# Kernel tuning notes

Measured on AMD Instinct MI355X. Metric: run time of the kernel, lower is better.

The kernel has to match this reference:

```python
import jax, jax.numpy as jnp
import numpy as np

S, T1, B = 1024, 65, 32   # source len, target len (incl. <start>), batch
E, H, V, D = 512, 512, 32000, 32  # embed, hidden, vocab, window half-width
PAD = 0


def _p(key, shape):
    return jax.random.normal(key, shape, dtype=jnp.float32) * 0.05


def setup_inputs() -> dict:
    key = jax.random.key(0)
    ks = jax.random.split(key, 16)
    return {
        "source": jax.random.randint(ks[0], (S, B), 0, V),
        "target": jax.random.randint(ks[1], (T1, B), 0, V),
        "src_emb": _p(ks[2], (V, E)),
        "tar_emb": _p(ks[3], (V, E)),
        "enc_Wih": _p(ks[4], (4 * H, E)),
        "enc_Whh": _p(ks[5], (4 * H, H)),
        "enc_b": _p(ks[6], (4 * H,)),
        "dec_Wih": _p(ks[7], (4 * H, E + H)),
        "dec_Whh": _p(ks[8], (4 * H, H)),
        "dec_b": _p(ks[9], (4 * H,)),
        "W_ht2tan": _p(ks[10], (H, H)),
        "W_tan2pt": _p(ks[11], (1, H)),
        "W_ct2ht": _p(ks[12], (H, 2 * H)),
        "W_ht2final": _p(ks[13], (V, H)),
    }


def _lstm_cell(x, h, c, Wih, Whh, b):
    g = x @ Wih.T + h @ Whh.T + b  # [B,4H], torch gate order i,f,g,o
    i, f, gg, o = jnp.split(g, 4, axis=-1)
    c = jax.nn.sigmoid(f) * c + jax.nn.sigmoid(i) * jnp.tanh(gg)
    h = jax.nn.sigmoid(o) * jnp.tanh(c)
    return h, c


def reference(source, target, src_emb, tar_emb, enc_Wih, enc_Whh, enc_b,
              dec_Wih, dec_Whh, dec_b, W_ht2tan, W_tan2pt, W_ct2ht, W_ht2final):
    # ---- encode (all lengths == S, so packing is a no-op) ----
    x = src_emb[source]  # [S,B,E]
    h0 = jnp.zeros((B, H), jnp.float32)

    def enc_step(carry, xt):
        h, c = carry
        h, c = _lstm_cell(xt, h, c, enc_Wih, enc_Whh, enc_b)
        return (h, c), h

    (hn, cn), enc_out = jax.lax.scan(enc_step, (h0, h0), x)
    encode_h = enc_out.transpose(1, 0, 2)  # [B,S,H]
    lens_f = jnp.full((B,), float(S), jnp.float32)
    pos = jnp.arange(S, dtype=jnp.float32)  # [S]

    # ---- decode ----
    y = tar_emb[target[:-1]]  # [T,B,E]

    def dec_step(carry, y_t):
        h, c, ht = carry
        x_t = jnp.concatenate([y_t, ht], axis=1)  # [B,E+H]
        h, c = _lstm_cell(x_t, h, c, dec_Wih, dec_Whh, dec_b)
        yt = h  # [B,H]
        pt = jax.nn.sigmoid(jnp.tanh(yt @ W_ht2tan.T) @ W_tan2pt.T)[:, 0]  # [B]
        center = lens_f * pt  # [B]
        ci = jnp.floor(center).astype(jnp.int32)
        left = jnp.maximum(0, ci - D)  # [B]
        right = jnp.minimum(S, ci + D)
        mask = (pos[None, :] >= left[:, None, None].squeeze(-1)) & (pos[None, :] < right[:, None])  # [B,S]
        scores = jnp.einsum('bh,bsh->bs', yt, encode_h)
        align = jax.nn.softmax(jnp.where(mask, scores, -1e30), axis=-1)
        gauss = jnp.exp(-jnp.square(pos[None, :] - center[:, None]) / (D * D / 2.0))
        at = align * gauss * mask
        ct = jnp.einsum('bs,bsh->bh', at, encode_h)
        # original computes attention under torch.no_grad()
        batch_ct = jax.lax.stop_gradient(jnp.concatenate([ct, yt], axis=1))  # [B,2H]
        ht_new = jnp.tanh(batch_ct @ W_ct2ht.T)
        return (h, c, ht_new), ht_new

    ht0 = jnp.zeros((B, H), jnp.float32)
    _, dec_out = jax.lax.scan(dec_step, (hn, cn, ht0), y)  # [T,B,H]

    P = jax.nn.log_softmax(dec_out @ W_ht2final.T, axis=-1)  # [T,B,V]
    tgt = target[1:]  # [T,B]
    tar_mask = (tgt != PAD).astype(jnp.float32)
    logp = jnp.take_along_axis(P, tgt[..., None], axis=-1)[..., 0] * tar_mask
    return logp.sum(axis=0)  # [B]
```

## Files before the change

### kernel.cpp

```cpp
#include <hip/hip_runtime.h>
#include <stdint.h>
#include <math.h>


typedef _Float16 f16;
typedef _Float16 f16x2 __attribute__((ext_vector_type(2)));
typedef _Float16 f16x4v __attribute__((ext_vector_type(4)));
typedef _Float16 f16x8v __attribute__((ext_vector_type(8)));
typedef float    f32x4v __attribute__((ext_vector_type(4)));
typedef int i32x4 __attribute__((ext_vector_type(4)));

union V8 { f16x2 p[4]; float4 f4; };

#define CH  4
#define WPC 64

__device__ __forceinline__ float dot2f(f16x2 a, f16x2 b, float c) {
#if __has_builtin(__builtin_amdgcn_fdot2)
    return __builtin_amdgcn_fdot2(a, b, c, false);
#else
    return c + (float)a[0] * (float)b[0] + (float)a[1] * (float)b[1];
#endif
}

__device__ __forceinline__ float sigf(float x) { return 1.0f / (1.0f + __expf(-x)); }

__device__ __forceinline__ float tanh_f(float x) {
    float ax = fminf(fabsf(x), 12.0f);
    float e  = __expf(2.0f * ax);
    float r  = (e - 1.0f) / (e + 1.0f);
    return copysignf(r, x);
}

__device__ __forceinline__ void st_wt_b16(f16* p, f16 v) {
    union { f16 h; uint16_t u; } cv; cv.h = v;
    uint32_t d = cv.u;
    asm volatile("global_store_short %0, %1, off sc0 sc1" :: "v"(p), "v"(d) : "memory");
}
__device__ __forceinline__ void st_wt_f32(float* p, float v) {
    union { float f; int i; } cv; cv.f = v;
    asm volatile("global_store_dword %0, %1, off sc0 sc1" :: "v"(p), "v"(cv.i) : "memory");
}
__device__ __forceinline__ void st_wt_b128(i32x4* p, i32x4 v) {
    asm volatile("global_store_dwordx4 %0, %1, off sc0 sc1" :: "v"(p), "v"(v) : "memory");
}
__device__ __forceinline__ i32x4 ld_bypass4(const void* p) {
    i32x4 v;
    asm volatile("global_load_dwordx4 %0, %1, off sc0 sc1\n\ts_waitcnt vmcnt(0)"
                 : "=v"(v) : "v"(p) : "memory");
    return v;
}
__device__ __forceinline__ unsigned ld_bypass_u32(const void* p) {
    unsigned v;
    asm volatile("global_load_dword %0, %1, off sc0 sc1\n\ts_waitcnt vmcnt(0)"
                 : "=v"(v) : "v"(p) : "memory");
    return v;
}

__device__ __forceinline__ bool chunk_ok(i32x4 v) {
    unsigned a = ~(unsigned)v[0], b = ~(unsigned)v[1];
    unsigned c = ~(unsigned)v[2], d = ~(unsigned)v[3];
    unsigned ok = (unsigned)((a & 0xFFFFu) != 0u) & (unsigned)((a >> 16) != 0u)
                & (unsigned)((b & 0xFFFFu) != 0u) & (unsigned)((b >> 16) != 0u)
                & (unsigned)((c & 0xFFFFu) != 0u) & (unsigned)((c >> 16) != 0u)
                & (unsigned)((d & 0xFFFFu) != 0u) & (unsigned)((d >> 16) != 0u);
    return ok != 0u;
}

__device__ __forceinline__ i32x4 poll16(const f16* gp) {
    i32x4 v = ld_bypass4(gp);
    while (!chunk_ok(v)) v = ld_bypass4(gp);
    return v;
}

__device__ __forceinline__ int rowp(int n) {
    return (((n & 31) >> 3) * 512) + ((n >> 5) * 8) + (n & 7);
}

__global__ void fill_sentinel(i32x4* h, i32x4* q, i32x4* c, i32x4* p,
                              float* se, float* tl) {
    const size_t NH = (size_t)CH * 1089 * 512;
    const size_t NQ = (size_t)CH * 65 * 512;
    const size_t NC = (size_t)64 * CH * 8 * 64;
    const size_t NP = (size_t)64 * CH * 8 * 16;
    const size_t total = NH + NQ + NC + NP;
    const i32x4 S = {-1, -1, -1, -1};
    const i32x4 Z = {0, 0, 0, 0};
    size_t stp = (size_t)gridDim.x * blockDim.x;
    for (size_t i = (size_t)blockIdx.x * blockDim.x + threadIdx.x; i < total; i += stp) {
        if (i < NH) {
            size_t r = i % (size_t)(1089 * 512);
            st_wt_b128(h + i, (r < 512) ? Z : S);
        } else if (i < NH + NQ) {
            size_t j = i - NH;
            size_t r = j % (size_t)(65 * 512);
            st_wt_b128(q + j, (r < 512) ? Z : S);
        } else if (i < NH + NQ + NC) {
            st_wt_b128(c + (i - NH - NQ), S);
        } else {
            st_wt_b128(p + (i - NH - NQ - NC), S);
        }
    }
    size_t g = (size_t)blockIdx.x * blockDim.x + threadIdx.x;
    if (g < 2048) { se[g] = 0.0f; tl[g] = 0.0f; }
}

__global__ void convert_weights(const float* __restrict__ encWhh,
                                const float* __restrict__ decWih,
                                const float* __restrict__ decWhh,
                                const float* __restrict__ ht2tan,
                                const float* __restrict__ ct2ht,
                                f16* __restrict__ Wenc, f16* __restrict__ Wdih,
                                f16* __restrict__ Wdhh, f16* __restrict__ T2l,
                                f16* __restrict__ CT2l) {
    const int NW = 2048 * 512;
    const int total = 3 * NW + 512 * 512 + 512 * 1024;
    int i = blockIdx.x * blockDim.x + threadIdx.x;
    int st = gridDim.x * blockDim.x;
    for (; i < total; i += st) {
        if (i < NW) {
            int n = i >> 9, k = i & 511;
            Wenc[i] = (f16)encWhh[rowp(n) * 512 + k];
        } else if (i < 2 * NW) {
            int j = i - NW; int n = j >> 9, k = j & 511;
            Wdih[j] = (f16)decWih[rowp(n) * 1024 + 512 + k];
        } else if (i < 3 * NW) {
            int j = i - 2 * NW; int n = j >> 9, k = j & 511;
            Wdhh[j] = (f16)decWhh[rowp(n) * 512 + k];
        } else if (i < 3 * NW + 512 * 512) {
            int j = i - 3 * NW;
            T2l[j] = (f16)ht2tan[j];
        } else {
            int j = i - 3 * NW - 512 * 512;
            CT2l[j] = (f16)ct2ht[j];
        }
    }
}

__global__ void convert_wfinal(const float* __restrict__ Wf, f16* __restrict__ Wh) {
    const int total = 32000 * 512;
    int i = blockIdx.x * blockDim.x + threadIdx.x;
    int st = gridDim.x * blockDim.x;
    for (; i < total; i += st) Wh[i] = (f16)Wf[i];
}

template <typename OutT>
__global__ __launch_bounds__(256) void gemm_gather(
    const float* __restrict__ emb, const int* __restrict__ idx,
    const float* __restrict__ W, int ldw,
    const float* __restrict__ bias, OutT* __restrict__ out) {
    __shared__ float As[16][65];
    __shared__ float Bs[16][65];
    const int tid = threadIdx.x;
    const int n0 = blockIdx.x * 64;
    const int r0 = blockIdx.y * 64;
    const int tx = tid & 15, ty = tid >> 4;
    const int lk = tid & 3,  lr = tid >> 2;
    const float* arow = emb + (size_t)idx[r0 + lr] * 512 + lk * 4;
    const float* brow = W + (size_t)rowp(n0 + lr) * ldw + lk * 4;
    float acc[4][4] = {};
    for (int k0 = 0; k0 < 512; k0 += 16) {
        float4 av = *(const float4*)(arow + k0);
        float4 bv = *(const float4*)(brow + k0);
        __syncthreads();
        As[lk * 4 + 0][lr] = av.x; As[lk * 4 + 1][lr] = av.y;
        As[lk * 4 + 2][lr] = av.z; As[lk * 4 + 3][lr] = av.w;
        Bs[lk * 4 + 0][lr] = bv.x; Bs[lk * 4 + 1][lr] = bv.y;
        Bs[lk * 4 + 2][lr] = bv.z; Bs[lk * 4 + 3][lr] = bv.w;
        __syncthreads();
#pragma unroll
        for (int k = 0; k < 16; k++) {
            float a4[4], b4[4];
#pragma unroll
            for (int i = 0; i < 4; i++) a4[i] = As[k][ty * 4 + i];
#pragma unroll
            for (int j = 0; j < 4; j++) b4[j] = Bs[k][tx * 4 + j];
#pragma unroll
            for (int i = 0; i < 4; i++)
#pragma unroll
                for (int j = 0; j < 4; j++) acc[i][j] = fmaf(a4[i], b4[j], acc[i][j]);
        }
    }
#pragma unroll
    for (int j = 0; j < 4; j++) {
        int n = n0 + tx * 4 + j;
        float bv2 = bias[rowp(n)];
#pragma unroll
        for (int i = 0; i < 4; i++) {
            int r = r0 + ty * 4 + i;
            int t = r >> 5, B = r & 31;
            size_t addr = ((((size_t)t * 4 + (B >> 3)) * 64 + (n >> 5)) * 32
                           + (n & 31)) * 8 + (B & 7);
            out[addr] = (OutT)(acc[i][j] + bv2);
        }
    }
}

__global__ __launch_bounds__(256) void gemm_eg_mfma(
    const float* __restrict__ emb, const int* __restrict__ idx,
    const float* __restrict__ W, const float* __restrict__ bias,
    f16* __restrict__ out) {
    __shared__ __align__(16) f16 Af[64][40];
    __shared__ __align__(16) f16 Bf[64][40];
    const int tid = threadIdx.x;
    const int n0 = blockIdx.x * 64;
    const int r0 = blockIdx.y * 64;
    const int srow = tid >> 2, sseg = tid & 3;
    const float* arow = emb + (size_t)idx[r0 + srow] * 512 + sseg * 8;
    const float* brow = W + (size_t)rowp(n0 + srow) * 512 + sseg * 8;
    const int w = tid >> 6, l = tid & 63;
    const int lr = l & 15, lk = l >> 4;
    f32x4v acc[4] = {};
    for (int k0 = 0; k0 < 512; k0 += 32) {
        float4 a0 = *(const float4*)(arow + k0);
        float4 a1 = *(const float4*)(arow + k0 + 4);
        float4 b0 = *(const float4*)(brow + k0);
        float4 b1 = *(const float4*)(brow + k0 + 4);
        __syncthreads();
        f16x8v av, bv;
        av[0]=(f16)a0.x; av[1]=(f16)a0.y; av[2]=(f16)a0.z; av[3]=(f16)a0.w;
        av[4]=(f16)a1.x; av[5]=(f16)a1.y; av[6]=(f16)a1.z; av[7]=(f16)a1.w;
        bv[0]=(f16)b0.x; bv[1]=(f16)b0.y; bv[2]=(f16)b0.z; bv[3]=(f16)b0.w;
        bv[4]=(f16)b1.x; bv[5]=(f16)b1.y; bv[6]=(f16)b1.z; bv[7]=(f16)b1.w;
        *(f16x8v*)&Af[srow][sseg * 8] = av;
        *(f16x8v*)&Bf[srow][sseg * 8] = bv;
        __syncthreads();
        f16x8v af = *(const f16x8v*)&Af[w * 16 + lr][lk * 8];
#pragma unroll
        for (int j = 0; j < 4; j++) {
            f16x8v bf = *(const f16x8v*)&Bf[j * 16 + lr][lk * 8];
            acc[j] = __builtin_amdgcn_mfma_f32_16x16x32_f16(af, bf, acc[j], 0, 0, 0);
        }
    }
    const int rq = r0 + w * 16 + lk * 4;
    const int t = rq >> 5;
    const int B = rq & 31;
#pragma unroll
    for (int j = 0; j < 4; j++) {
        int n = n0 + j * 16 + lr;
        float bb = bias[rowp(n)];
        f16x4v pk;
#pragma unroll
        for (int r = 0; r < 4; r++) pk[r] = (f16)(acc[j][r] + bb);
        size_t addr = ((((size_t)t * 4 + (B >> 3)) * 64 + (n >> 5)) * 32
                       + (n & 31)) * 8 + (B & 7);
        *(f16x4v*)(out + addr) = pk;
    }
}

__global__ __launch_bounds__(256) void proj_lse_mfma(
    const f16* __restrict__ A, const f16* __restrict__ Wh,
    const int* __restrict__ target,
    float* __restrict__ se, float* __restrict__ tl) {
    __shared__ __align__(16) f16 Af[64][40];
    __shared__ __align__(16) f16 Bf[64][40];
    const int tid = threadIdx.x;
    const int v0 = blockIdx.x * 64;
    const int r0 = blockIdx.y * 64;
    const int srow = tid >> 2, sseg = tid & 3;
    const f16* arow = A + (size_t)(r0 + srow) * 512 + sseg * 8;
    const f16* brow = Wh + (size_t)(v0 + srow) * 512 + sseg * 8;
    const int w = tid >> 6, l = tid & 63;
    const int lr = l & 15, lk = l >> 4;
    f32x4v acc[4] = {};
    for (int k0 = 0; k0 < 512; k0 += 32) {
        f16x8v av = *(const f16x8v*)(arow + k0);
        f16x8v bv = *(const f16x8v*)(brow + k0);
        __syncthreads();
        *(f16x8v*)&Af[srow][sseg * 8] = av;
        *(f16x8v*)&Bf[srow][sseg * 8] = bv;
        __syncthreads();
        f16x8v af = *(const f16x8v*)&Af[w * 16 + lr][lk * 8];
#pragma unroll
        for (int j = 0; j < 4; j++) {
            f16x8v bf = *(const f16x8v*)&Bf[j * 16 + lr][lk * 8];
            acc[j] = __builtin_amdgcn_mfma_f32_16x16x32_f16(af, bf, acc[j], 0, 0, 0);
        }
    }
#pragma unroll
    for (int r = 0; r < 4; r++) {
        int rg = r0 + w * 16 + lk * 4 + r;
        int tg = target[32 + rg];
        float es = 0.0f;
#pragma unroll
        for (int j = 0; j < 4; j++) {
            int n = v0 + j * 16 + lr;
            float lv = acc[j][r];
            if (n == tg) atomicAdd(&tl[rg], lv);
            es += __expf(lv);
        }
#pragma unroll
        for (int m = 1; m < 16; m <<= 1) es += __shfl_xor(es, m);
        if (lr == 0) atomicAdd(&se[rg], es);
    }
}

__global__ __launch_bounds__(512, 2) void scan_kernel(
    const f16* __restrict__ eg,
    const float* __restrict__ dg,
    const f16* __restrict__ Wenc,
    const f16* __restrict__ Wdih,
    const f16* __restrict__ Wdhh,
    const f16* __restrict__ T2l,
    const f16* __restrict__ CT2l,
    const float* __restrict__ wpt,
    f16* __restrict__ h_hist,
    f16* __restrict__ q_hist,
    f16* __restrict__ ctb,
    float* __restrict__ ppart,
    f16* __restrict__ dout) {
    const int bid = blockIdx.x;
    const int chain = bid >> 6;
    const int wg = bid & 63;
    const int tid = threadIdx.x;

    f16* hc = h_hist + (size_t)chain * 1089 * 4096;
    f16* qc = q_hist + (size_t)chain * 65 * 4096;

    __shared__ __align__(16) f16  Ws[32 * 520];
    __shared__ __align__(16) f16  hst[8 * 520];
    __shared__ __align__(16) f16  qst[8 * 520];
    __shared__ __align__(16) f16  yst[8 * 520];
    __shared__ __align__(16) f16  ctst[8 * 520];
    __shared__ float part[512];
    __shared__ float zbS[64];
    __shared__ float spart[64 * 9];
    __shared__ float scS[64];
    __shared__ float atwS[64];
    __shared__ float ptS[1];

    const int c  = (tid >> 3) & 31;
    const int bq = tid & 7;
    const int kh = tid >> 8;
    const int sb = tid >> 6, sj = tid & 63;
    const int au = tid & 7, ab = tid >> 3;

    {
        int r = tid >> 4, seg = tid & 15;
        const float4* s4 = (const float4*)(Wenc + (size_t)(wg * 32 + r) * 512) + seg * 4;
        float4 a0 = s4[0], a1 = s4[1], a2 = s4[2], a3 = s4[3];
        float4* d4 = (float4*)(Ws + r * 520) + seg * 4;
        d4[0] = a0; d4[1] = a1; d4[2] = a2; d4[3] = a3;
    }
    __syncthreads();

    V8 wreg[32];
    {
        const f16* Wr = Ws + c * 520 + kh * 256;
#pragma unroll
        for (int k8 = 0; k8 < 32; k8++) wreg[k8].f4 = *(const float4*)(Wr + k8 * 8);
    }

    float creg = 0.0f;

    float egv = 0.0f;
    if (kh == 0)
        egv = (float)eg[(size_t)chain * 16384 + wg * 256 + c * 8 + bq];

    for (int t = 0; t < 1024; t++) {
        {
            i32x4 v = poll16(hc + (size_t)t * 4096 + sb * 512 + sj * 8);
            *((i32x4*)(hst + sb * 520) + sj) = v;
        }
        float egn = 0.0f;
        if (kh == 0 && t < 1023)
            egn = (float)eg[((size_t)(t + 1) * 4 + chain) * 16384 + wg * 256 + c * 8 + bq];
        __syncthreads();
        {
            const f16* hr = hst + bq * 520 + kh * 256;
            float a0 = (kh == 0) ? egv : 0.0f;
#pragma unroll
            for (int k8 = 0; k8 < 32; k8++) {
                V8 xv;
                xv.f4 = *(const float4*)(hr + k8 * 8);
#pragma unroll
                for (int q = 0; q < 4; q++) a0 = dot2f(wreg[k8].p[q], xv.p[q], a0);
            }
            part[tid] = a0;
        }
        egv = egn;
        __syncthreads();
        if (tid < 64) {
            float gi = part[(au)      * 8 + ab] + part[256 + (au)      * 8 + ab];
            float gf = part[(8 + au)  * 8 + ab] + part[256 + (8 + au)  * 8 + ab];
            float gg = part[(16 + au) * 8 + ab] + part[256 + (16 + au) * 8 + ab];
            float go = part[(24 + au) * 8 + ab] + part[256 + (24 + au) * 8 + ab];
            float cc = sigf(gf) * creg + sigf(gi) * tanh_f(gg);
            float hh = sigf(go) * tanh_f(cc);
            creg = cc;
            st_wt_b16(hc + (size_t)(t + 1) * 4096 + ab * 512 + wg * 8 + au, (f16)hh);
        }
    }

    {
        const f16* W1 = Wdih + (size_t)(wg * 32 + c) * 512 + kh * 256;
#pragma unroll
        for (int k8 = 0; k8 < 32; k8++) wreg[k8].f4 = *(const float4*)(W1 + k8 * 8);
    }
    {
        i32x4 v = poll16(hc + (size_t)1024 * 4096 + sb * 512 + sj * 8);
        *((i32x4*)(yst + sb * 520) + sj) = v;
    }

    for (int t = 0; t < 64; t++) {
        f16* ydst = hc + (size_t)(1025 + t) * 4096;

        {
            i32x4 v = poll16(qc + (size_t)t * 4096 + sb * 512 + sj * 8);
            *((i32x4*)(qst + sb * 520) + sj) = v;
        }
        __syncthreads();
        {
            float dgv = (kh == 0)
                ? dg[((size_t)t * 4 + chain) * 16384 + wg * 256 + c * 8 + bq] : 0.0f;
            const f16* W2 = Wdhh + (size_t)(wg * 32 + c) * 512 + kh * 256;
            const f16* q0 = qst + bq * 520 + kh * 256;
            const f16* h0 = yst + bq * 520 + kh * 256;
            float a0 = dgv;
#pragma unroll
            for (int k8 = 0; k8 < 32; k8++) {
                V8 w2, x0, y0;
                x0.f4 = *(const float4*)(q0 + k8 * 8);
                w2.f4 = *(const float4*)(W2 + k8 * 8);
                y0.f4 = *(const float4*)(h0 + k8 * 8);
#pragma unroll
                for (int q = 0; q < 4; q++) {
                    a0 = dot2f(wreg[k8].p[q], x0.p[q], a0);
                    a0 = dot2f(w2.p[q], y0.p[q], a0);
                }
            }
            part[tid] = a0;
        }
        __syncthreads();
        if (tid < 64) {
            float gi = part[(au)      * 8 + ab] + part[256 + (au)      * 8 + ab];
            float gf = part[(8 + au)  * 8 + ab] + part[256 + (8 + au)  * 8 + ab];
            float gg = part[(16 + au) * 8 + ab] + part[256 + (16 + au) * 8 + ab];
            float go = part[(24 + au) * 8 + ab] + part[256 + (24 + au) * 8 + ab];
            float cc = sigf(gf) * creg + sigf(gi) * tanh_f(gg);
            float hh = sigf(go) * tanh_f(cc);
            creg = cc;
            st_wt_b16(ydst + ab * 512 + wg * 8 + au, (f16)hh);
        }

        {
            i32x4 v = poll16(ydst + sb * 512 + sj * 8);
            *((i32x4*)(yst + sb * 520) + sj) = v;
        }
        __syncthreads();
        {
            int kq = tid >> 6, zu = (tid >> 3) & 7, zq = tid & 7;
            const f16* Tr = T2l + (size_t)(wg * 8 + zu) * 512 + kq * 64;
            const f16* yr = yst + zq * 520 + kq * 64;
            float s = 0.0f;
#pragma unroll
            for (int k = 0; k < 64; k += 8) {
                V8 aa, bb;
                aa.f4 = *(const float4*)(Tr + k);
                bb.f4 = *(const float4*)(yr + k);
#pragma unroll
                for (int q = 0; q < 4; q++) s = dot2f(aa.p[q], bb.p[q], s);
            }
            part[tid] = s;
        }
        __syncthreads();
        if (tid < 64) {
            float z = 0.0f;
#pragma unroll
            for (int kq = 0; kq < 8; kq++) z += part[kq * 64 + tid];
            zbS[tid] = tanh_f(z);
        }
        __syncthreads();
        if (tid < 8) {
            float pp = 0.0f;
#pragma unroll
            for (int u2 = 0; u2 < 8; u2++) pp += zbS[u2 * 8 + tid] * wpt[wg * 8 + u2];
            st_wt_f32(&ppart[(((size_t)t * 4 + chain) * 8 + tid) * 64 + wg], pp);
        }

        if (wg < 8) {
            const int bb = wg;
            if (tid < 64) {
                const float* pa = ppart + (((size_t)t * 4 + chain) * 8 + bb) * 64 + tid;
                unsigned bits = ld_bypass_u32(pa);
                while (bits == 0xFFFFFFFFu) bits = ld_bypass_u32(pa);
                union { unsigned u; float f; } cv; cv.u = bits;
                float v = cv.f;
#pragma unroll
                for (int off = 32; off > 0; off >>= 1) v += __shfl_down(v, off);
                if (tid == 0) ptS[0] = v;
            }
            __syncthreads();
            float pt = sigf(ptS[0]);
            float center = 1024.0f * pt;
            int ci = (int)floorf(center);
            int left = max(0, ci - 32);
            int right = min(1024, ci + 32);
            int win = right - left;
            int p = tid >> 3, seg = tid & 7;
            if (p < win) {
                const f16* yr = yst + bb * 520 + seg * 64;
                const f16* er = hc + (size_t)(left + p + 1) * 4096 + bb * 512 + seg * 64;
                float s = 0.0f;
#pragma unroll
                for (int k = 0; k < 64; k += 8) {
                    V8 aa, bbv;
                    aa.f4  = *(const float4*)(yr + k);
                    bbv.f4 = *(const float4*)(er + k);
#pragma unroll
                    for (int q = 0; q < 4; q++) s = dot2f(aa.p[q], bbv.p[q], s);
                }
                spart[p * 9 + seg] = s;
            }
            __syncthreads();
            if (tid < 64) {
                float s = -1e30f;
                if (tid < win) {
                    s = 0.0f;
#pragma unroll
                    for (int x = 0; x < 8; x++) s += spart[tid * 9 + x];
                }
                scS[tid] = s;
            }
            __syncthreads();
            float mx = -1e30f;
            for (int q2 = 0; q2 < 64; q2++) mx = fmaxf(mx, scS[q2]);
            float sum = 0.0f;
            for (int q2 = 0; q2 < 64; q2++) sum += __expf(scS[q2] - mx);
            if (tid < 64) {
                float sp = (float)(left + tid) - center;
                float gs = __expf(-(sp * sp) * (1.0f / 512.0f));
                atwS[tid] = (tid < win) ? (__expf(scS[tid] - mx) / sum) * gs : 0.0f;
            }
            __syncthreads();
            {
                int j = tid;
                float a = 0.0f;
                const f16* ebase = hc + (size_t)(left + 1) * 4096 + bb * 512 + j;
                for (int p2 = 0; p2 < win; p2++)
                    a += atwS[p2] * (float)ebase[(size_t)p2 * 4096];
                st_wt_b16(ctb + ((((size_t)t * 4 + chain) * 8 + bb) * 512) + j, (f16)a);
            }
        }

        {
            i32x4 v = poll16(ctb + (((size_t)t * 4 + chain) * 8 + sb) * 512 + sj * 8);
            *((i32x4*)(ctst + sb * 520) + sj) = v;
        }
        __syncthreads();
        {
            int kq = tid >> 6, du = (tid >> 3) & 7, dq = tid & 7;
            const f16* Cr = CT2l + (size_t)(wg * 8 + du) * 1024 + kq * 128;
            const f16* xr = (kq < 4)
                ? (ctst + dq * 520 + kq * 128)
                : (yst + dq * 520 + (kq - 4) * 128);
            float s = 0.0f;
#pragma unroll 4
            for (int k = 0; k < 128; k += 8) {
                V8 aa, bb;
                aa.f4 = *(const float4*)(Cr + k);
                bb.f4 = *(const float4*)(xr + k);
#pragma unroll
                for (int q = 0; q < 4; q++) s = dot2f(aa.p[q], bb.p[q], s);
            }
            part[tid] = s;
        }
        __syncthreads();
        if (tid < 64) {
            float s = 0.0f;
#pragma unroll
            for (int kq = 0; kq < 8; kq++) s += part[kq * 64 + tid];
            float hv = tanh_f(s);
            int du = tid >> 3, dq = tid & 7;
            st_wt_b16(qc + (size_t)(t + 1) * 4096 + dq * 512 + wg * 8 + du, (f16)hv);
            dout[((size_t)t * 32 + chain * 8 + dq) * 512 + wg * 8 + du] = (f16)hv;
        }
    }
}

__global__ void finalize_out(const float* __restrict__ se, const float* __restrict__ tl,
                             const int* __restrict__ target, float* __restrict__ out) {
    int b = threadIdx.x;
    if (b >= 32) return;
    float s = 0.0f;
    for (int t = 0; t < 64; t++) {
        int r = t * 32 + b;
        int tg = target[(t + 1) * 32 + b];
        if (tg != 0) s += tl[r] - logf(se[r]);
    }
    out[b] = s;
}

extern "C" void kernel_launch(void* const* d_in, const int* in_sizes, int n_in,
                              void* d_out, int out_size, void* d_ws, size_t ws_size,
                              hipStream_t stream) {
    const int*   source   = (const int*)  d_in[0];
    const int*   target   = (const int*)  d_in[1];
    const float* src_emb  = (const float*)d_in[2];
    const float* tar_emb  = (const float*)d_in[3];
    const float* enc_Wih  = (const float*)d_in[4];
    const float* enc_Whh  = (const float*)d_in[5];
    const float* enc_b    = (const float*)d_in[6];
    const float* dec_Wih  = (const float*)d_in[7];
    const float* dec_Whh  = (const float*)d_in[8];
    const float* dec_b    = (const float*)d_in[9];
    const float* W_ht2tan = (const float*)d_in[10];
    const float* W_tan2pt = (const float*)d_in[11];
    const float* W_ct2ht  = (const float*)d_in[12];
    const float* W_final  = (const float*)d_in[13];
    float* out = (float*)d_out;

    char* ws = (char*)d_ws;
    size_t off = 0;
    auto alloc = [&](size_t bytes) -> char* {
        char* p = ws + off;
        off = (off + bytes + 255) & ~(size_t)255;
        return p;
    };
    f16*   h_hist = (f16*)  alloc((size_t)CH * 1089 * 4096 * 2);
    f16*   q_hist = (f16*)  alloc((size_t)CH * 65 * 4096 * 2);
    f16*   ctb    = (f16*)  alloc((size_t)64 * CH * 8 * 512 * 2);
    float* ppart  = (float*)alloc((size_t)64 * CH * 8 * 64 * 4);
    float* se     = (float*)alloc((size_t)2048 * 4);
    float* tl     = (float*)alloc((size_t)2048 * 4);
    f16*   eg     = (f16*)  alloc((size_t)32768 * 2048 * 2);
    float* dg     = (float*)alloc((size_t)2048 * 2048 * 4);
    f16*   Wenc   = (f16*)  alloc((size_t)2048 * 512 * 2);
    f16*   Wdih   = (f16*)  alloc((size_t)2048 * 512 * 2);
    f16*   Wdhh   = (f16*)  alloc((size_t)2048 * 512 * 2);
    f16*   T2l    = (f16*)  alloc((size_t)512 * 512 * 2);
    f16*   CT2l   = (f16*)  alloc((size_t)512 * 1024 * 2);
    f16*   dout   = (f16*)  alloc((size_t)2048 * 512 * 2);
    f16*   Wf16   = eg;

    fill_sentinel<<<2048, 256, 0, stream>>>((i32x4*)h_hist, (i32x4*)q_hist,
                                            (i32x4*)ctb, (i32x4*)ppart, se, tl);
    convert_weights<<<2048, 256, 0, stream>>>(enc_Whh, dec_Wih, dec_Whh, W_ht2tan, W_ct2ht,
                                              Wenc, Wdih, Wdhh, T2l, CT2l);
    gemm_eg_mfma<<<dim3(32, 512), 256, 0, stream>>>(src_emb, source, enc_Wih, enc_b, eg);
    gemm_gather<float><<<dim3(32, 32), 256, 0, stream>>>(tar_emb, target, dec_Wih, 1024,
                                                         dec_b, dg);
    scan_kernel<<<CH * WPC, 512, 0, stream>>>(eg, dg, Wenc, Wdih, Wdhh, T2l, CT2l,
                                              W_tan2pt, h_hist, q_hist, ctb, ppart,
                                              dout);
    convert_wfinal<<<2048, 256, 0, stream>>>(W_final, Wf16);
    proj_lse_mfma<<<dim3(500, 32), 256, 0, stream>>>(dout, Wf16, target, se, tl);
    finalize_out<<<1, 64, 0, stream>>>(se, tl, target, out);
}
```

Before: 5.931 ms.

## Use MFMA in a single wave for encoder recurrence with double-buffered hidden state

The encoder LSTM step's per-thread fdot2 reductions over 512 threads are replaced by a single wavefront issuing 16x16x32 f16 MFMAs, with weights held as MFMA A-fragments in registers. The hidden-state staging buffer is double-buffered and zero-padded to 16 rows, which removes one of the two block barriers per step. The input-gate preactivations are prefetched per lane for all four gates. This shortens the serial per-timestep latency, at the cost of idling most of the block during the matmul and wasting half the MFMA columns on padding.

```diff
diff --git a/kernel.cpp b/kernel.cpp
--- a/kernel.cpp
+++ b/kernel.cpp
@@ -318,7 +318,7 @@
     f16* qc = q_hist + (size_t)chain * 65 * 4096;
 
     __shared__ __align__(16) f16  Ws[32 * 520];
-    __shared__ __align__(16) f16  hst[8 * 520];
+    __shared__ __align__(16) f16  hb[2 * 16 * 520];
     __shared__ __align__(16) f16  qst[8 * 520];
     __shared__ __align__(16) f16  yst[8 * 520];
     __shared__ __align__(16) f16  ctst[8 * 520];
@@ -342,60 +342,75 @@
         float4* d4 = (float4*)(Ws + r * 520) + seg * 4;
         d4[0] = a0; d4[1] = a1; d4[2] = a2; d4[3] = a3;
     }
+    {
+        const i32x4 Z = {0, 0, 0, 0};
+        for (int i = tid; i < 2 * 16 * 520 / 8; i += 512) ((i32x4*)hb)[i] = Z;
+    }
     __syncthreads();
 
-    V8 wreg[32];
-    {
-        const f16* Wr = Ws + c * 520 + kh * 256;
-#pragma unroll
-        for (int k8 = 0; k8 < 32; k8++) wreg[k8].f4 = *(const float4*)(Wr + k8 * 8);
-    }
+    const int l    = tid & 63;
+    const int lr16 = l & 15, lkc = l >> 4;
+    f16x8v af[2][16];
+#pragma unroll
+    for (int m = 0; m < 2; m++)
+#pragma unroll
+        for (int kk = 0; kk < 16; kk++)
+            af[m][kk] = *(const f16x8v*)(Ws + (size_t)(m * 16 + lr16) * 520
+                                            + kk * 32 + lkc * 8);
 
     float creg = 0.0f;
-
-    float egv = 0.0f;
-    if (kh == 0)
-        egv = (float)eg[(size_t)chain * 16384 + wg * 256 + c * 8 + bq];
+    f16 eg4[4] = {(f16)0.0f, (f16)0.0f, (f16)0.0f, (f16)0.0f};
+    if (tid < 64) {
+#pragma unroll
+        for (int g = 0; g < 4; g++)
+            eg4[g] = eg[(size_t)chain * 16384 + wg * 256 + (g * 8 + au) * 8 + ab];
+    }
 
     for (int t = 0; t < 1024; t++) {
+        f16* hbuf = hb + (t & 1) * (16 * 520);
         {
             i32x4 v = poll16(hc + (size_t)t * 4096 + sb * 512 + sj * 8);
-            *((i32x4*)(hst + sb * 520) + sj) = v;
-        }
-        float egn = 0.0f;
-        if (kh == 0 && t < 1023)
-            egn = (float)eg[((size_t)(t + 1) * 4 + chain) * 16384 + wg * 256 + c * 8 + bq];
-        __syncthreads();
-        {
-            const f16* hr = hst + bq * 520 + kh * 256;
-            float a0 = (kh == 0) ? egv : 0.0f;
-#pragma unroll
-            for (int k8 = 0; k8 < 32; k8++) {
-                V8 xv;
-                xv.f4 = *(const float4*)(hr + k8 * 8);
-#pragma unroll
-                for (int q = 0; q < 4; q++) a0 = dot2f(wreg[k8].p[q], xv.p[q], a0);
-            }
-            part[tid] = a0;
-        }
-        egv = egn;
+            *((i32x4*)(hbuf + sb * 520) + sj) = v;
+        }
         __syncthreads();
         if (tid < 64) {
-            float gi = part[(au)      * 8 + ab] + part[256 + (au)      * 8 + ab];
-            float gf = part[(8 + au)  * 8 + ab] + part[256 + (8 + au)  * 8 + ab];
-            float gg = part[(16 + au) * 8 + ab] + part[256 + (16 + au) * 8 + ab];
-            float go = part[(24 + au) * 8 + ab] + part[256 + (24 + au) * 8 + ab];
+            f32x4v acc0 = {}, acc1 = {};
+#pragma unroll
+            for (int kk = 0; kk < 16; kk++) {
+                f16x8v bf = *(const f16x8v*)(hbuf + (size_t)lr16 * 520
+                                                  + kk * 32 + lkc * 8);
+                acc0 = __builtin_amdgcn_mfma_f32_16x16x32_f16(af[0][kk], bf, acc0, 0, 0, 0);
+                acc1 = __builtin_amdgcn_mfma_f32_16x16x32_f16(af[1][kk], bf, acc1, 0, 0, 0);
+            }
+            if (lr16 < 8) {
+#pragma unroll
+                for (int r = 0; r < 4; r++) {
+                    part[(lkc * 4 + r) * 8 + lr16]      = acc0[r];
+                    part[(16 + lkc * 4 + r) * 8 + lr16] = acc1[r];
+                }
+            }
+            float gi = (float)eg4[0] + part[(au) * 8 + ab];
+            float gf = (float)eg4[1] + part[(8 + au) * 8 + ab];
+            float gg = (float)eg4[2] + part[(16 + au) * 8 + ab];
+            float go = (float)eg4[3] + part[(24 + au) * 8 + ab];
             float cc = sigf(gf) * creg + sigf(gi) * tanh_f(gg);
             float hh = sigf(go) * tanh_f(cc);
             creg = cc;
             st_wt_b16(hc + (size_t)(t + 1) * 4096 + ab * 512 + wg * 8 + au, (f16)hh);
-        }
-    }
-
+            if (t < 1023) {
+#pragma unroll
+                for (int g = 0; g < 4; g++)
+                    eg4[g] = eg[((size_t)(t + 1) * 4 + chain) * 16384
+                                + wg * 256 + (g * 8 + au) * 8 + ab];
+            }
+        }
+    }
+
+    V8 wregD[32];
     {
         const f16* W1 = Wdih + (size_t)(wg * 32 + c) * 512 + kh * 256;
 #pragma unroll
-        for (int k8 = 0; k8 < 32; k8++) wreg[k8].f4 = *(const float4*)(W1 + k8 * 8);
+        for (int k8 = 0; k8 < 32; k8++) wregD[k8].f4 = *(const float4*)(W1 + k8 * 8);
     }
     {
         i32x4 v = poll16(hc + (size_t)1024 * 4096 + sb * 512 + sj * 8);
@@ -425,7 +440,7 @@
                 y0.f4 = *(const float4*)(h0 + k8 * 8);
 #pragma unroll
                 for (int q = 0; q < 4; q++) {
-                    a0 = dot2f(wreg[k8].p[q], x0.p[q], a0);
+                    a0 = dot2f(wregD[k8].p[q], x0.p[q], a0);
                     a0 = dot2f(w2.p[q], y0.p[q], a0);
                 }
             }
```

Measured after the change: 5.384 ms. -9.2%, faster.
